# Optimization experiments

Measured on AMD Instinct MI355X. Metric: run time of the kernel, lower is better.

## Reference

```python
import jax, jax.numpy as jnp
import numpy as np
from jax import lax


def _binarize(t):
    # sign binarization to +1/-1 (zero maps to -1, matching torch.where(t > 0, 1, -1))
    return jnp.where(t > 0, 1.0, -1.0).astype(t.dtype)


def _bconv(x, w, b):
    # binary conv: binarize input and weights, then standard 3x3 'same' conv
    y = lax.conv_general_dilated(
        _binarize(x), _binarize(w),
        window_strides=(1, 1), padding=((1, 1), (1, 1)),
        dimension_numbers=('NCHW', 'OIHW', 'NCHW'))
    return y + b[None, :, None, None]


def _maxpool2(x):
    return lax.reduce_window(x, -jnp.inf, lax.max, (1, 1, 2, 2), (1, 1, 2, 2), 'VALID')


def setup_inputs() -> dict:
    key = jax.random.key(0)
    ks = jax.random.split(key, 13)
    s = 0.1
    return {
        'x': jax.random.normal(ks[0], (4096, 1, 28, 28), jnp.float32),
        'w1': jax.random.normal(ks[1], (32, 1, 3, 3), jnp.float32) * s,
        'b1': jax.random.normal(ks[2], (32,), jnp.float32) * s,
        'w2': jax.random.normal(ks[3], (64, 32, 3, 3), jnp.float32) * s,
        'b2': jax.random.normal(ks[4], (64,), jnp.float32) * s,
        'w3': jax.random.normal(ks[5], (16, 64, 3, 3), jnp.float32) * s,
        'b3': jax.random.normal(ks[6], (16,), jnp.float32) * s,
        'fc1_w': jax.random.normal(ks[7], (256, 16 * 7 * 7), jnp.float32) * s,
        'fc1_b': jax.random.normal(ks[8], (256,), jnp.float32) * s,
        'fc2_w': jax.random.normal(ks[9], (128, 256), jnp.float32) * s,
        'fc2_b': jax.random.normal(ks[10], (128,), jnp.float32) * s,
        'fc3_w': jax.random.normal(ks[11], (10, 128), jnp.float32) * s,
        'fc3_b': jax.random.normal(ks[12], (10,), jnp.float32) * s,
    }


def reference(x, w1, b1, w2, b2, w3, b3, fc1_w, fc1_b, fc2_w, fc2_b, fc3_w, fc3_b):
    h = jax.nn.relu(_maxpool2(_bconv(x, w1, b1)))      # [B,32,14,14]
    h = jax.nn.relu(_maxpool2(_bconv(h, w2, b2)))      # [B,64,7,7]
    h = jax.nn.relu(_bconv(h, w3, b3))                 # [B,16,7,7]
    h = h.reshape(-1, 16 * 7 * 7)
    h = jax.nn.relu(h @ fc1_w.T + fc1_b)
    h = jax.nn.relu(h @ fc2_w.T + fc2_b)
    return h @ fc3_w.T + fc3_b                          # [B,10]
```

## Files before the change

kernel.cpp:

```cpp
#include <hip/hip_runtime.h>
#include <cstdint>

#define OFF_PW    0
#define OFF_W1T   4096
#define OFF_W2T   823296
#define OFF_H3T   954368
#define OFF_H1T   14061568
#define OFF_H2T   18255872

__global__ __launch_bounds__(256) void prep(
    const float* __restrict__ w1, const float* __restrict__ w2,
    const float* __restrict__ w3,
    const float* __restrict__ fc1_w, const float* __restrict__ fc2_w,
    uint32_t* __restrict__ pw, float* __restrict__ w1T, float* __restrict__ w2T) {
    int t = threadIdx.x;
    if (blockIdx.x == 0) {
        if (t < 32) {
            uint32_t b = 0;
            for (int k = 0; k < 9; ++k) b |= (w1[t * 9 + k] > 0.f ? 1u : 0u) << k;
            pw[t] = b;
        }
        for (int idx = t; idx < 576; idx += 256) {
            int oc = idx / 9, tap = idx % 9;
            int kh = tap / 3, kw = tap % 3;
            uint32_t b = 0;
            for (int ic = 0; ic < 32; ++ic)
                b |= (w2[((oc * 32 + ic) * 3 + kh) * 3 + kw] > 0.f ? 1u : 0u) << ic;
            pw[32 + idx] = b;
        }
        for (int idx = t; idx < 144; idx += 256) {
            int oc = idx / 9, tap = idx % 9;
            int kh = tap / 3, kw = tap % 3;
            uint32_t lo = 0, hi = 0;
            for (int ic = 0; ic < 32; ++ic) {
                lo |= (w3[((oc * 64 + ic) * 3 + kh) * 3 + kw] > 0.f ? 1u : 0u) << ic;
                hi |= (w3[((oc * 64 + ic + 32) * 3 + kh) * 3 + kw] > 0.f ? 1u : 0u) << ic;
            }
            pw[608 + idx * 2] = lo;
            pw[608 + idx * 2 + 1] = hi;
        }
    } else {
        int e = (blockIdx.x - 1) * 256 + t;
        if (e < 204800) {
            int k = e >> 8, n = e & 255;
            w1T[e] = (k < 784) ? fc1_w[n * 784 + k] : 0.f;
        } else {
            int e2 = e - 204800;
            int k = e2 >> 7, n = e2 & 127;
            w2T[e2] = fc2_w[n * 256 + k];
        }
    }
}

__global__ __launch_bounds__(256) void conv_stack(
    const float* __restrict__ x,
    const float* __restrict__ b1, const float* __restrict__ b2,
    const float* __restrict__ b3,
    const uint32_t* __restrict__ pw,
    float* __restrict__ h3T) {
    __shared__ uint32_t s_wb1[32];
    __shared__ uint32_t s_W2[576];
    __shared__ uint32_t s_W3[288];
    __shared__ float s_b1[32], s_b2[64], s_b3[16];
    __shared__ uint32_t s_xrow[28];
    __shared__ uint32_t s_H1[256];
    __shared__ uint32_t s_H2[162];

    const int t = threadIdx.x;
    const int img = blockIdx.x;

    s_H1[t] = 0;
    if (t < 162) s_H2[t] = 0;
    if (t < 32) { s_wb1[t] = pw[t]; s_b1[t] = b1[t]; }
    if (t >= 32 && t < 96) s_b2[t - 32] = b2[t - 32];
    if (t >= 96 && t < 112) s_b3[t - 96] = b3[t - 96];
    for (int i = t; i < 576; i += 256) s_W2[i] = pw[32 + i];
    for (int i = t; i < 288; i += 256) s_W3[i] = pw[608 + i];
    if (t >= 192 && t < 220) {
        int r = t - 192;
        const float* xr = x + img * 784 + r * 28;
        uint32_t b = 0;
        for (int j = 0; j < 28; ++j) b |= (xr[j] > 0.f ? 1u : 0u) << j;
        s_xrow[r] = b;
    }
    __syncthreads();

    if (t < 196) {
        int pi = t / 14, pj = t % 14;
        uint32_t sarr[4], marr[4];
        int pcm[4];
#pragma unroll
        for (int p = 0; p < 4; ++p) {
            int i = 2 * pi + (p >> 1), j = 2 * pj + (p & 1);
            uint32_t sb = 0, mb = 0;
            int bit = 0;
#pragma unroll
            for (int di = -1; di <= 1; ++di) {
                int y = i + di;
                bool rv = (unsigned)y < 28u;
                uint32_t row = rv ? s_xrow[rv ? y : 0] : 0u;
#pragma unroll
                for (int dj = -1; dj <= 1; ++dj) {
                    int xx = j + dj;
                    bool v = rv && (unsigned)xx < 28u;
                    if (v) {
                        mb |= 1u << bit;
                        sb |= ((row >> xx) & 1u) << bit;
                    }
                    ++bit;
                }
            }
            sarr[p] = sb; marr[p] = mb; pcm[p] = __popc(mb);
        }
        uint32_t word = 0;
#pragma unroll
        for (int c = 0; c < 32; ++c) {
            uint32_t w = s_wb1[c];
            int best = -1000;
#pragma unroll
            for (int p = 0; p < 4; ++p) {
                int v = pcm[p] - 2 * __popc((sarr[p] ^ w) & marr[p]);
                best = v > best ? v : best;
            }
            word |= ((float)best + s_b1[c] > 0.f ? 1u : 0u) << c;
        }
        s_H1[(pi + 1) * 16 + (pj + 1)] = word;
    }
    __syncthreads();

    for (int task = t; task < 400; task += 256) {
        int q = task / 25, ip = task - q * 25;
        int pi = ip / 5 + 1, pj = ip % 5 + 1;
        uint32_t cell[16];
#pragma unroll
        for (int r = 0; r < 4; ++r)
#pragma unroll
            for (int c = 0; c < 4; ++c)
                cell[r * 4 + c] = s_H1[(2 * pi + r) * 16 + (2 * pj + c)];
        uint32_t nib = 0;
#pragma unroll
        for (int o = 0; o < 4; ++o) {
            int oc = q * 4 + o;
            const uint32_t* wrow = &s_W2[oc * 9];
            int best = -100000;
#pragma unroll
            for (int a = 0; a < 2; ++a)
#pragma unroll
                for (int b = 0; b < 2; ++b) {
                    int S = 0;
#pragma unroll
                    for (int kh = 0; kh < 3; ++kh)
#pragma unroll
                        for (int kw = 0; kw < 3; ++kw)
                            S += __popc(cell[(a + kh) * 4 + (b + kw)] ^ wrow[kh * 3 + kw]);
                    int v = 288 - 2 * S;
                    best = v > best ? v : best;
                }
            nib |= ((float)best + s_b2[oc] > 0.f ? 1u : 0u) << (oc & 31);
        }
        atomicOr((unsigned int*)&s_H2[((pi + 1) * 9 + (pj + 1)) * 2 + (q >> 3)],
                 (unsigned int)nib);
    }
    for (int task = t; task < 384; task += 256) {
        int q = task / 24, bp = task - q * 24;
        int pi, pj;
        if (bp < 7)       { pi = 0; pj = bp; }
        else if (bp < 14) { pi = 6; pj = bp - 7; }
        else if (bp < 19) { pi = bp - 13; pj = 0; }
        else              { pi = bp - 18; pj = 6; }
        uint32_t vr[4], vc[4];
#pragma unroll
        for (int r = 0; r < 4; ++r) {
            vr[r] = ((unsigned)(2 * pi - 1 + r) < 14u) ? 0xFFFFFFFFu : 0u;
            vc[r] = ((unsigned)(2 * pj - 1 + r) < 14u) ? 0xFFFFFFFFu : 0u;
        }
        uint32_t cell[16], V[16];
#pragma unroll
        for (int r = 0; r < 4; ++r)
#pragma unroll
            for (int c = 0; c < 4; ++c) {
                cell[r * 4 + c] = s_H1[(2 * pi + r) * 16 + (2 * pj + c)];
                V[r * 4 + c] = vr[r] & vc[c];
            }
        int nvp[4];
#pragma unroll
        for (int a = 0; a < 2; ++a)
#pragma unroll
            for (int b = 0; b < 2; ++b) {
                int i = 2 * pi + a, j = 2 * pj + b;
                int vy = 3 - (i == 0) - (i == 13);
                int vx = 3 - (j == 0) - (j == 13);
                nvp[a * 2 + b] = 32 * vy * vx;
            }
        uint32_t nib = 0;
#pragma unroll
        for (int o = 0; o < 4; ++o) {
            int oc = q * 4 + o;
            const uint32_t* wrow = &s_W2[oc * 9];
            int best = -100000;
#pragma unroll
            for (int a = 0; a < 2; ++a)
#pragma unroll
                for (int b = 0; b < 2; ++b) {
                    int S = 0;
#pragma unroll
                    for (int kh = 0; kh < 3; ++kh)
#pragma unroll
                        for (int kw = 0; kw < 3; ++kw) {
                            int ci = (a + kh) * 4 + (b + kw);
                            S += __popc((cell[ci] ^ wrow[kh * 3 + kw]) & V[ci]);
                        }
                    int v = nvp[a * 2 + b] - 2 * S;
                    best = v > best ? v : best;
                }
            nib |= ((float)best + s_b2[oc] > 0.f ? 1u : 0u) << (oc & 31);
        }
        atomicOr((unsigned int*)&s_H2[((pi + 1) * 9 + (pj + 1)) * 2 + (q >> 3)],
                 (unsigned int)nib);
    }
    __syncthreads();

    for (int task = t; task < 784; task += 256) {
        int oc = task / 49, pos = task - oc * 49;
        int pi = pos / 7, pj = pos % 7;
        uint32_t vr[3], vc[3];
#pragma unroll
        for (int d = 0; d < 3; ++d) {
            vr[d] = ((unsigned)(pi - 1 + d) < 7u) ? 0xFFFFFFFFu : 0u;
            vc[d] = ((unsigned)(pj - 1 + d) < 7u) ? 0xFFFFFFFFu : 0u;
        }
        int vy = 3 - (pi == 0) - (pi == 6);
        int vx = 3 - (pj == 0) - (pj == 6);
        int Nv = 64 * vy * vx;
        const uint32_t* wr = &s_W3[oc * 18];
        int S = 0;
#pragma unroll
        for (int kh = 0; kh < 3; ++kh)
#pragma unroll
            for (int kw = 0; kw < 3; ++kw) {
                uint32_t V = vr[kh] & vc[kw];
                int idx = ((pi + kh) * 9 + (pj + kw)) * 2;
                S += __popc((s_H2[idx] ^ wr[(kh * 3 + kw) * 2]) & V);
                S += __popc((s_H2[idx + 1] ^ wr[(kh * 3 + kw) * 2 + 1]) & V);
            }
        float h = (float)(Nv - 2 * S) + s_b3[oc];
        h3T[task * 4096 + img] = h > 0.f ? h : 0.f;
    }
}

__global__ __launch_bounds__(256) void fc1_gemm(
    const float* __restrict__ aT,
    const float* __restrict__ bT,
    const float* __restrict__ bias,
    float* __restrict__ oT) {
    const int KC = 80, LD = 68;
    __shared__ float As[KC * LD];
    __shared__ float Bs[KC * LD];
    const int t = threadIdx.x;
    const int tx = t & 15, ty = t >> 4;
    const int img0 = blockIdx.x * 64;
    const int n0 = blockIdx.y * 64;
    float acc[4][4] = {{0.f}};

    for (int kc = 0; kc < 800; kc += KC) {
#pragma unroll
        for (int s = 0; s < 5; ++s) {
            int v = t + s * 256;
            int kk = v >> 4, i4 = (v & 15) * 4;
            *(float4*)&As[kk * LD + i4] =
                *(const float4*)&aT[(kc + kk) * 4096 + img0 + i4];
            *(float4*)&Bs[kk * LD + i4] =
                *(const float4*)&bT[(kc + kk) * 256 + n0 + i4];
        }
        __syncthreads();
#pragma unroll 4
        for (int kk = 0; kk < KC; ++kk) {
            float4 a = *(const float4*)&As[kk * LD + ty * 4];
            float4 b = *(const float4*)&Bs[kk * LD + tx * 4];
            acc[0][0] += a.x * b.x; acc[0][1] += a.x * b.y;
            acc[0][2] += a.x * b.z; acc[0][3] += a.x * b.w;
            acc[1][0] += a.y * b.x; acc[1][1] += a.y * b.y;
            acc[1][2] += a.y * b.z; acc[1][3] += a.y * b.w;
            acc[2][0] += a.z * b.x; acc[2][1] += a.z * b.y;
            acc[2][2] += a.z * b.z; acc[2][3] += a.z * b.w;
            acc[3][0] += a.w * b.x; acc[3][1] += a.w * b.y;
            acc[3][2] += a.w * b.z; acc[3][3] += a.w * b.w;
        }
        __syncthreads();
    }
    float4 bb = *(const float4*)&bias[n0 + tx * 4];
    float bv[4] = {bb.x, bb.y, bb.z, bb.w};
#pragma unroll
    for (int jj = 0; jj < 4; ++jj) {
        float4 ov;
        ov.x = acc[0][jj] + bv[jj]; ov.x = ov.x > 0.f ? ov.x : 0.f;
        ov.y = acc[1][jj] + bv[jj]; ov.y = ov.y > 0.f ? ov.y : 0.f;
        ov.z = acc[2][jj] + bv[jj]; ov.z = ov.z > 0.f ? ov.z : 0.f;
        ov.w = acc[3][jj] + bv[jj]; ov.w = ov.w > 0.f ? ov.w : 0.f;
        *(float4*)&oT[(n0 + tx * 4 + jj) * 4096 + img0 + ty * 4] = ov;
    }
}

__global__ __launch_bounds__(256) void fc2_gemm(
    const float* __restrict__ aT,
    const float* __restrict__ bT,
    const float* __restrict__ bias,
    float* __restrict__ oT) {
    const int KC = 64, LDA = 68, LDB = 36;
    __shared__ float As[KC * LDA];
    __shared__ float Bs[KC * LDB];
    const int t = threadIdx.x;
    const int tx = t & 15, ty = t >> 4;
    const int img0 = blockIdx.x * 64;
    const int n0 = blockIdx.y * 32;
    float acc[4][2] = {{0.f}};

    for (int kc = 0; kc < 256; kc += KC) {
#pragma unroll
        for (int s = 0; s < 4; ++s) {
            int v = t + s * 256;
            int kk = v >> 4, i4 = (v & 15) * 4;
            *(float4*)&As[kk * LDA + i4] =
                *(const float4*)&aT[(kc + kk) * 4096 + img0 + i4];
        }
#pragma unroll
        for (int s = 0; s < 2; ++s) {
            int v = t + s * 256;
            int kk = v >> 3, n4 = (v & 7) * 4;
            *(float4*)&Bs[kk * LDB + n4] =
                *(const float4*)&bT[(kc + kk) * 128 + n0 + n4];
        }
        __syncthreads();
#pragma unroll 4
        for (int kk = 0; kk < KC; ++kk) {
            float4 a = *(const float4*)&As[kk * LDA + ty * 4];
            float2 b = *(const float2*)&Bs[kk * LDB + tx * 2];
            acc[0][0] += a.x * b.x; acc[0][1] += a.x * b.y;
            acc[1][0] += a.y * b.x; acc[1][1] += a.y * b.y;
            acc[2][0] += a.z * b.x; acc[2][1] += a.z * b.y;
            acc[3][0] += a.w * b.x; acc[3][1] += a.w * b.y;
        }
        __syncthreads();
    }
#pragma unroll
    for (int j = 0; j < 2; ++j) {
        int n = n0 + tx * 2 + j;
        float bj = bias[n];
        float4 ov;
        ov.x = acc[0][j] + bj; ov.x = ov.x > 0.f ? ov.x : 0.f;
        ov.y = acc[1][j] + bj; ov.y = ov.y > 0.f ? ov.y : 0.f;
        ov.z = acc[2][j] + bj; ov.z = ov.z > 0.f ? ov.z : 0.f;
        ov.w = acc[3][j] + bj; ov.w = ov.w > 0.f ? ov.w : 0.f;
        *(float4*)&oT[n * 4096 + img0 + ty * 4] = ov;
    }
}

__global__ __launch_bounds__(256) void fc3_gemm(
    const float* __restrict__ aT,
    const float* __restrict__ w,
    const float* __restrict__ bias,
    float* __restrict__ out) {
    int id = blockIdx.x * 256 + threadIdx.x;
    int n = id >> 12, img = id & 4095;
    const float* wr = w + n * 128;
    float a0 = 0.f, a1 = 0.f, a2 = 0.f, a3 = 0.f;
#pragma unroll 8
    for (int k = 0; k < 128; k += 4) {
        a0 += aT[(k + 0) * 4096 + img] * wr[k + 0];
        a1 += aT[(k + 1) * 4096 + img] * wr[k + 1];
        a2 += aT[(k + 2) * 4096 + img] * wr[k + 2];
        a3 += aT[(k + 3) * 4096 + img] * wr[k + 3];
    }
    out[img * 10 + n] = (a0 + a1) + (a2 + a3) + bias[n];
}

extern "C" void kernel_launch(void* const* d_in, const int* in_sizes, int n_in,
                              void* d_out, int out_size, void* d_ws, size_t ws_size,
                              hipStream_t stream) {
    const float* x     = (const float*)d_in[0];
    const float* w1    = (const float*)d_in[1];
    const float* b1    = (const float*)d_in[2];
    const float* w2    = (const float*)d_in[3];
    const float* b2    = (const float*)d_in[4];
    const float* w3    = (const float*)d_in[5];
    const float* b3    = (const float*)d_in[6];
    const float* fc1_w = (const float*)d_in[7];
    const float* fc1_b = (const float*)d_in[8];
    const float* fc2_w = (const float*)d_in[9];
    const float* fc2_b = (const float*)d_in[10];
    const float* fc3_w = (const float*)d_in[11];
    const float* fc3_b = (const float*)d_in[12];
    float* out = (float*)d_out;

    const int B = in_sizes[0] / 784;
    char* ws = (char*)d_ws;
    uint32_t* pw = (uint32_t*)(ws + OFF_PW);
    float* w1T = (float*)(ws + OFF_W1T);
    float* w2T = (float*)(ws + OFF_W2T);
    float* h3T = (float*)(ws + OFF_H3T);
    float* h1T = (float*)(ws + OFF_H1T);
    float* h2T = (float*)(ws + OFF_H2T);

    hipLaunchKernelGGL(prep, dim3(929), dim3(256), 0, stream,
                       w1, w2, w3, fc1_w, fc2_w, pw, w1T, w2T);
    hipLaunchKernelGGL(conv_stack, dim3(B), dim3(256), 0, stream,
                       x, b1, b2, b3, pw, h3T);
    hipLaunchKernelGGL(fc1_gemm, dim3(B / 64, 4), dim3(256), 0, stream,
                       h3T, w1T, fc1_b, h1T);
    hipLaunchKernelGGL(fc2_gemm, dim3(B / 64, 4), dim3(256), 0, stream,
                       h1T, w2T, fc2_b, h2T);
    hipLaunchKernelGGL(fc3_gemm, dim3(B * 10 / 256), dim3(256), 0, stream,
                       h2T, fc3_w, fc3_b, out);
}
```

Baseline: 219.7 us.

## Process one image per wavefront in conv stack with padded bit layout and precomputed thresholds

The conv stack now maps one image to each 64-lane wavefront, four images per block, each with its own padded bit buffers in shared memory. Conv1 reads bits from a zero-padded row layout, and conv2 gives one output channel to each lane with register-held weights, packing results with a ballot instead of shared atomics. Bias comparisons become integer thresholds, and border padding corrections come from tables built in prep. The table lives in the h1T workspace region, which fc1 later overwrites. Interior tiles run fewer bitwise ops, but wavefronts loop sequentially over positions.

```diff
diff --git a/kernel.cpp b/kernel.cpp
--- a/kernel.cpp
+++ b/kernel.cpp
@@ -1,24 +1,45 @@
 #include <hip/hip_runtime.h>
 #include <cstdint>
 
-#define OFF_PW    0
 #define OFF_W1T   4096
 #define OFF_W2T   823296
 #define OFF_H3T   954368
 #define OFF_H1T   14061568
 #define OFF_H2T   18255872
 
+#define TW_WB1    0
+#define TW_W2     32
+#define TW_W3     608
+#define TW_CORR2  896
+#define TW_CORR3  1920
+#define TW_TLE1   2176
+#define TW_TGE1   2208
+#define TW_TLE2   2240
+#define TW_TGE2   2304
+
+__device__ __forceinline__ int imin2(int a, int b) { return a < b ? a : b; }
+__device__ __forceinline__ int imax2(int a, int b) { return a > b ? a : b; }
+
 __global__ __launch_bounds__(256) void prep(
-    const float* __restrict__ w1, const float* __restrict__ w2,
+    const float* __restrict__ w1, const float* __restrict__ b1,
+    const float* __restrict__ w2, const float* __restrict__ b2,
     const float* __restrict__ w3,
     const float* __restrict__ fc1_w, const float* __restrict__ fc2_w,
-    uint32_t* __restrict__ pw, float* __restrict__ w1T, float* __restrict__ w2T) {
+    int* __restrict__ tab, float* __restrict__ w1T, float* __restrict__ w2T) {
     int t = threadIdx.x;
+    uint32_t* utab = (uint32_t*)tab;
     if (blockIdx.x == 0) {
         if (t < 32) {
             uint32_t b = 0;
             for (int k = 0; k < 9; ++k) b |= (w1[t * 9 + k] > 0.f ? 1u : 0u) << k;
-            pw[t] = b;
+            utab[TW_WB1 + t] = b;
+            tab[TW_TLE1 + t] = (int)floorf((9.f + b1[t]) * 0.5f);
+            tab[TW_TGE1 + t] = (int)floorf(-b1[t]) + 1;
+        }
+        if (t >= 32 && t < 96) {
+            int oc = t - 32;
+            tab[TW_TLE2 + oc] = (int)floorf((288.f + b2[oc]) * 0.5f);
+            tab[TW_TGE2 + oc] = (int)floorf(-b2[oc]) + 1;
         }
         for (int idx = t; idx < 576; idx += 256) {
             int oc = idx / 9, tap = idx % 9;
@@ -26,18 +47,46 @@
             uint32_t b = 0;
             for (int ic = 0; ic < 32; ++ic)
                 b |= (w2[((oc * 32 + ic) * 3 + kh) * 3 + kw] > 0.f ? 1u : 0u) << ic;
-            pw[32 + idx] = b;
-        }
-        for (int idx = t; idx < 144; idx += 256) {
-            int oc = idx / 9, tap = idx % 9;
+            utab[TW_W2 + idx] = b;
+        }
+        for (int idx = t; idx < 288; idx += 256) {
+            int oc = idx / 18, rem = idx % 18;
+            int tap = rem >> 1, word = rem & 1;
             int kh = tap / 3, kw = tap % 3;
-            uint32_t lo = 0, hi = 0;
-            for (int ic = 0; ic < 32; ++ic) {
-                lo |= (w3[((oc * 64 + ic) * 3 + kh) * 3 + kw] > 0.f ? 1u : 0u) << ic;
-                hi |= (w3[((oc * 64 + ic + 32) * 3 + kh) * 3 + kw] > 0.f ? 1u : 0u) << ic;
-            }
-            pw[608 + idx * 2] = lo;
-            pw[608 + idx * 2 + 1] = hi;
+            uint32_t b = 0;
+            for (int ic = 0; ic < 32; ++ic)
+                b |= (w3[((oc * 64 + ic + 32 * word) * 3 + kh) * 3 + kw] > 0.f ? 1u : 0u) << ic;
+            utab[TW_W3 + idx] = b;
+        }
+        __syncthreads();
+        for (int idx = t; idx < 1024; idx += 256) {
+            int pat = idx >> 6, oc = idx & 63;
+            int s = 0, n = 0;
+            for (int tap = 0; tap < 9; ++tap) {
+                int kh = tap / 3, kw = tap % 3;
+                bool pad = ((pat & 1) && kh == 0) || ((pat & 2) && kh == 2) ||
+                           ((pat & 4) && kw == 0) || ((pat & 8) && kw == 2);
+                if (pad) { s += __popc(utab[TW_W2 + oc * 9 + tap]); ++n; }
+            }
+            tab[TW_CORR2 + idx] = 2 * s - 32 * n;
+        }
+        {
+            int idx = t;
+            if (idx < 256) {
+                int pat = idx >> 4, oc = idx & 15;
+                int s = 0, n = 0;
+                for (int tap = 0; tap < 9; ++tap) {
+                    int kh = tap / 3, kw = tap % 3;
+                    bool pad = ((pat & 1) && kh == 0) || ((pat & 2) && kh == 2) ||
+                               ((pat & 4) && kw == 0) || ((pat & 8) && kw == 2);
+                    if (pad) {
+                        s += __popc(utab[TW_W3 + oc * 18 + tap * 2]) +
+                             __popc(utab[TW_W3 + oc * 18 + tap * 2 + 1]);
+                        ++n;
+                    }
+                }
+                tab[TW_CORR3 + idx] = 2 * s - 64 * n;
+            }
         }
     } else {
         int e = (blockIdx.x - 1) * 256 + t;
@@ -52,199 +101,236 @@
     }
 }
 
-__global__ __launch_bounds__(256) void conv_stack(
+#define WV_SIZE 456
+
+__global__ __launch_bounds__(256, 6) void conv_stack(
     const float* __restrict__ x,
-    const float* __restrict__ b1, const float* __restrict__ b2,
     const float* __restrict__ b3,
-    const uint32_t* __restrict__ pw,
+    const int* __restrict__ tab,
     float* __restrict__ h3T) {
-    __shared__ uint32_t s_wb1[32];
-    __shared__ uint32_t s_W2[576];
-    __shared__ uint32_t s_W3[288];
-    __shared__ float s_b1[32], s_b2[64], s_b3[16];
-    __shared__ uint32_t s_xrow[28];
-    __shared__ uint32_t s_H1[256];
-    __shared__ uint32_t s_H2[162];
-
+    __shared__ uint32_t SH[4 * WV_SIZE];
     const int t = threadIdx.x;
-    const int img = blockIdx.x;
-
-    s_H1[t] = 0;
-    if (t < 162) s_H2[t] = 0;
-    if (t < 32) { s_wb1[t] = pw[t]; s_b1[t] = b1[t]; }
-    if (t >= 32 && t < 96) s_b2[t - 32] = b2[t - 32];
-    if (t >= 96 && t < 112) s_b3[t - 96] = b3[t - 96];
-    for (int i = t; i < 576; i += 256) s_W2[i] = pw[32 + i];
-    for (int i = t; i < 288; i += 256) s_W3[i] = pw[608 + i];
-    if (t >= 192 && t < 220) {
-        int r = t - 192;
-        const float* xr = x + img * 784 + r * 28;
+    const int wid = t >> 6, lane = t & 63;
+    const int img = blockIdx.x * 4 + wid;
+    uint32_t* W = SH + wid * WV_SIZE;
+    const uint32_t* utab = (const uint32_t*)tab;
+
+#pragma unroll
+    for (int k = 0; k < 8; ++k) {
+        int idx = lane + k * 64;
+        if (idx < WV_SIZE) W[idx] = 0;
+    }
+
+    if (lane < 28) {
+        const float* xr = x + img * 784 + lane * 28;
         uint32_t b = 0;
-        for (int j = 0; j < 28; ++j) b |= (xr[j] > 0.f ? 1u : 0u) << j;
-        s_xrow[r] = b;
+#pragma unroll
+        for (int q = 0; q < 7; ++q) {
+            float4 v = *(const float4*)(xr + q * 4);
+            b |= (v.x > 0.f ? 1u : 0u) << (q * 4 + 0);
+            b |= (v.y > 0.f ? 1u : 0u) << (q * 4 + 1);
+            b |= (v.z > 0.f ? 1u : 0u) << (q * 4 + 2);
+            b |= (v.w > 0.f ? 1u : 0u) << (q * 4 + 3);
+        }
+        W[1 + lane] = b << 1;
     }
     __syncthreads();
 
-    if (t < 196) {
-        int pi = t / 14, pj = t % 14;
-        uint32_t sarr[4], marr[4];
+    for (int it = 0; it < 3; ++it) {
+        int p = it * 64 + lane;
+        bool act = p < 144;
+        int pp = act ? p : 0;
+        int Pi = 1 + pp / 12, Pj = 1 + pp % 12;
+        int i0 = 2 * Pi, j0 = 2 * Pj;
+        uint32_t r0 = W[i0], r1 = W[i0 + 1], r2 = W[i0 + 2], r3 = W[i0 + 3];
+        uint32_t f0a = (r0 >> j0) & 7, f0b = (r0 >> (j0 + 1)) & 7;
+        uint32_t f1a = (r1 >> j0) & 7, f1b = (r1 >> (j0 + 1)) & 7;
+        uint32_t f2a = (r2 >> j0) & 7, f2b = (r2 >> (j0 + 1)) & 7;
+        uint32_t f3a = (r3 >> j0) & 7, f3b = (r3 >> (j0 + 1)) & 7;
+        uint32_t s00 = f0a | (f1a << 3) | (f2a << 6);
+        uint32_t s01 = f0b | (f1b << 3) | (f2b << 6);
+        uint32_t s10 = f1a | (f2a << 3) | (f3a << 6);
+        uint32_t s11 = f1b | (f2b << 3) | (f3b << 6);
+        uint32_t word = 0;
+#pragma unroll
+        for (int oc = 0; oc < 32; ++oc) {
+            uint32_t w = utab[TW_WB1 + oc];
+            int m0 = __popc(s00 ^ w), m1 = __popc(s01 ^ w);
+            int m2 = __popc(s10 ^ w), m3 = __popc(s11 ^ w);
+            int mn = imin2(imin2(m0, m1), imin2(m2, m3));
+            word |= (mn <= tab[TW_TLE1 + oc] ? 1u : 0u) << oc;
+        }
+        if (act) W[32 + (Pi + 1) * 16 + (Pj + 1)] = word;
+    }
+    {
+        int p = lane;
+        bool act = p < 52;
+        int pp = act ? p : 28;
+        int Pi, Pj;
+        if (pp < 14)      { Pi = 0;  Pj = pp; }
+        else if (pp < 28) { Pi = 13; Pj = pp - 14; }
+        else if (pp < 40) { Pi = pp - 28 + 1; Pj = 0; }
+        else              { Pi = pp - 40 + 1; Pj = 13; }
+        int i0 = 2 * Pi, j0 = 2 * Pj;
+        uint32_t r0 = W[i0], r1 = W[i0 + 1], r2 = W[i0 + 2], r3 = W[i0 + 3];
+        uint32_t f0a = (r0 >> j0) & 7, f0b = (r0 >> (j0 + 1)) & 7;
+        uint32_t f1a = (r1 >> j0) & 7, f1b = (r1 >> (j0 + 1)) & 7;
+        uint32_t f2a = (r2 >> j0) & 7, f2b = (r2 >> (j0 + 1)) & 7;
+        uint32_t f3a = (r3 >> j0) & 7, f3b = (r3 >> (j0 + 1)) & 7;
+        uint32_t smp[4];
+        smp[0] = f0a | (f1a << 3) | (f2a << 6);
+        smp[1] = f0b | (f1b << 3) | (f2b << 6);
+        smp[2] = f1a | (f2a << 3) | (f3a << 6);
+        smp[3] = f1b | (f2b << 3) | (f3b << 6);
+        uint32_t mb[4];
         int pcm[4];
 #pragma unroll
-        for (int p = 0; p < 4; ++p) {
-            int i = 2 * pi + (p >> 1), j = 2 * pj + (p & 1);
-            uint32_t sb = 0, mb = 0;
-            int bit = 0;
-#pragma unroll
-            for (int di = -1; di <= 1; ++di) {
-                int y = i + di;
-                bool rv = (unsigned)y < 28u;
-                uint32_t row = rv ? s_xrow[rv ? y : 0] : 0u;
-#pragma unroll
-                for (int dj = -1; dj <= 1; ++dj) {
-                    int xx = j + dj;
-                    bool v = rv && (unsigned)xx < 28u;
-                    if (v) {
-                        mb |= 1u << bit;
-                        sb |= ((row >> xx) & 1u) << bit;
+        for (int a = 0; a < 2; ++a) {
+            int i = 2 * Pi + a;
+            uint32_t vre = 0x1FF;
+            if (i == 0)  vre &= ~0x007u;
+            if (i == 27) vre &= ~0x1C0u;
+#pragma unroll
+            for (int bb = 0; bb < 2; ++bb) {
+                int j = 2 * Pj + bb;
+                uint32_t vce = 0x1FF;
+                if (j == 0)  vce &= ~0x049u;
+                if (j == 27) vce &= ~0x124u;
+                mb[a * 2 + bb] = vre & vce;
+                pcm[a * 2 + bb] = __popc(vre & vce);
+            }
+        }
+        uint32_t word = 0;
+#pragma unroll
+        for (int oc = 0; oc < 32; ++oc) {
+            uint32_t w = utab[TW_WB1 + oc];
+            int best = -1000;
+#pragma unroll
+            for (int p4 = 0; p4 < 4; ++p4) {
+                int v = pcm[p4] - 2 * __popc((smp[p4] ^ w) & mb[p4]);
+                best = imax2(best, v);
+            }
+            word |= (best >= tab[TW_TGE1 + oc] ? 1u : 0u) << oc;
+        }
+        if (act) W[32 + (Pi + 1) * 16 + (Pj + 1)] = word;
+    }
+    __syncthreads();
+
+    {
+        uint32_t w2r[9];
+#pragma unroll
+        for (int k = 0; k < 9; ++k) w2r[k] = utab[TW_W2 + lane * 9 + k];
+        const int tle2 = tab[TW_TLE2 + lane];
+        const int tge2 = tab[TW_TGE2 + lane];
+        const uint32_t* H1 = W + 32;
+        uint32_t* H2 = W + 288;
+
+        for (int Pi = 1; Pi <= 5; ++Pi) {
+            for (int Pj = 1; Pj <= 5; ++Pj) {
+                uint32_t c[16];
+#pragma unroll
+                for (int r = 0; r < 4; ++r) {
+                    uint2 lo = *(const uint2*)&H1[(2 * Pi + r) * 16 + 2 * Pj];
+                    uint2 hi = *(const uint2*)&H1[(2 * Pi + r) * 16 + 2 * Pj + 2];
+                    c[r * 4 + 0] = lo.x; c[r * 4 + 1] = lo.y;
+                    c[r * 4 + 2] = hi.x; c[r * 4 + 3] = hi.y;
+                }
+                int Sv[4];
+#pragma unroll
+                for (int a = 0; a < 2; ++a)
+#pragma unroll
+                    for (int bb = 0; bb < 2; ++bb) {
+                        int s = 0;
+#pragma unroll
+                        for (int kh = 0; kh < 3; ++kh)
+#pragma unroll
+                            for (int kw = 0; kw < 3; ++kw)
+                                s += __popc(c[(a + kh) * 4 + (bb + kw)] ^ w2r[kh * 3 + kw]);
+                        Sv[a * 2 + bb] = s;
                     }
-                    ++bit;
+                int mn = imin2(imin2(Sv[0], Sv[1]), imin2(Sv[2], Sv[3]));
+                uint64_t bal = __ballot(mn <= tle2);
+                if (lane == 0) {
+                    uint2 wv = make_uint2((uint32_t)bal, (uint32_t)(bal >> 32));
+                    *(uint2*)&H2[((Pi + 1) * 9 + (Pj + 1)) * 2] = wv;
                 }
             }
-            sarr[p] = sb; marr[p] = mb; pcm[p] = __popc(mb);
-        }
-        uint32_t word = 0;
-#pragma unroll
-        for (int c = 0; c < 32; ++c) {
-            uint32_t w = s_wb1[c];
-            int best = -1000;
-#pragma unroll
-            for (int p = 0; p < 4; ++p) {
-                int v = pcm[p] - 2 * __popc((sarr[p] ^ w) & marr[p]);
-                best = v > best ? v : best;
-            }
-            word |= ((float)best + s_b1[c] > 0.f ? 1u : 0u) << c;
-        }
-        s_H1[(pi + 1) * 16 + (pj + 1)] = word;
+        }
+        for (int bp = 0; bp < 24; ++bp) {
+            int Pi, Pj;
+            if (bp < 7)       { Pi = 0; Pj = bp; }
+            else if (bp < 14) { Pi = 6; Pj = bp - 7; }
+            else if (bp < 19) { Pi = bp - 14 + 1; Pj = 0; }
+            else              { Pi = bp - 19 + 1; Pj = 6; }
+            uint32_t c[16];
+#pragma unroll
+            for (int r = 0; r < 4; ++r) {
+                uint2 lo = *(const uint2*)&H1[(2 * Pi + r) * 16 + 2 * Pj];
+                uint2 hi = *(const uint2*)&H1[(2 * Pi + r) * 16 + 2 * Pj + 2];
+                c[r * 4 + 0] = lo.x; c[r * 4 + 1] = lo.y;
+                c[r * 4 + 2] = hi.x; c[r * 4 + 3] = hi.y;
+            }
+            int Sv[4];
+#pragma unroll
+            for (int a = 0; a < 2; ++a)
+#pragma unroll
+                for (int bb = 0; bb < 2; ++bb) {
+                    int s = 0;
+#pragma unroll
+                    for (int kh = 0; kh < 3; ++kh)
+#pragma unroll
+                        for (int kw = 0; kw < 3; ++kw)
+                            s += __popc(c[(a + kh) * 4 + (bb + kw)] ^ w2r[kh * 3 + kw]);
+                    Sv[a * 2 + bb] = s;
+                }
+            int best = -100000;
+#pragma unroll
+            for (int a = 0; a < 2; ++a)
+#pragma unroll
+                for (int bb = 0; bb < 2; ++bb) {
+                    int i = 2 * Pi + a, j = 2 * Pj + bb;
+                    int pat = (i == 0 ? 1 : 0) | (i == 13 ? 2 : 0) |
+                              (j == 0 ? 4 : 0) | (j == 13 ? 8 : 0);
+                    int D = 288 - 2 * Sv[a * 2 + bb] + tab[TW_CORR2 + pat * 64 + lane];
+                    best = imax2(best, D);
+                }
+            uint64_t bal = __ballot(best >= tge2);
+            if (lane == 0) {
+                uint2 wv = make_uint2((uint32_t)bal, (uint32_t)(bal >> 32));
+                *(uint2*)&H2[((Pi + 1) * 9 + (Pj + 1)) * 2] = wv;
+            }
+        }
     }
     __syncthreads();
 
-    for (int task = t; task < 400; task += 256) {
-        int q = task / 25, ip = task - q * 25;
-        int pi = ip / 5 + 1, pj = ip % 5 + 1;
-        uint32_t cell[16];
-#pragma unroll
-        for (int r = 0; r < 4; ++r)
-#pragma unroll
-            for (int c = 0; c < 4; ++c)
-                cell[r * 4 + c] = s_H1[(2 * pi + r) * 16 + (2 * pj + c)];
-        uint32_t nib = 0;
-#pragma unroll
-        for (int o = 0; o < 4; ++o) {
-            int oc = q * 4 + o;
-            const uint32_t* wrow = &s_W2[oc * 9];
-            int best = -100000;
-#pragma unroll
-            for (int a = 0; a < 2; ++a)
-#pragma unroll
-                for (int b = 0; b < 2; ++b) {
-                    int S = 0;
-#pragma unroll
-                    for (int kh = 0; kh < 3; ++kh)
-#pragma unroll
-                        for (int kw = 0; kw < 3; ++kw)
-                            S += __popc(cell[(a + kh) * 4 + (b + kw)] ^ wrow[kh * 3 + kw]);
-                    int v = 288 - 2 * S;
-                    best = v > best ? v : best;
+    {
+        const uint32_t* H2 = W + 288;
+        int oc = lane & 15, sub = lane >> 4;
+        uint32_t w3r[18];
+#pragma unroll
+        for (int k = 0; k < 18; ++k) w3r[k] = utab[TW_W3 + oc * 18 + k];
+        float bias3 = b3[oc];
+        for (int g = 0; g < 13; ++g) {
+            int pos = g * 4 + sub;
+            bool act = pos < 49;
+            int pp = act ? pos : 0;
+            int Pi = pp / 7, Pj = pp % 7;
+            int s = 0;
+#pragma unroll
+            for (int kh = 0; kh < 3; ++kh)
+#pragma unroll
+                for (int kw = 0; kw < 3; ++kw) {
+                    uint2 hv = *(const uint2*)&H2[((Pi + kh) * 9 + (Pj + kw)) * 2];
+                    s += __popc(hv.x ^ w3r[(kh * 3 + kw) * 2]) +
+                         __popc(hv.y ^ w3r[(kh * 3 + kw) * 2 + 1]);
                 }
-            nib |= ((float)best + s_b2[oc] > 0.f ? 1u : 0u) << (oc & 31);
-        }
-        atomicOr((unsigned int*)&s_H2[((pi + 1) * 9 + (pj + 1)) * 2 + (q >> 3)],
-                 (unsigned int)nib);
-    }
-    for (int task = t; task < 384; task += 256) {
-        int q = task / 24, bp = task - q * 24;
-        int pi, pj;
-        if (bp < 7)       { pi = 0; pj = bp; }
-        else if (bp < 14) { pi = 6; pj = bp - 7; }
-        else if (bp < 19) { pi = bp - 13; pj = 0; }
-        else              { pi = bp - 18; pj = 6; }
-        uint32_t vr[4], vc[4];
-#pragma unroll
-        for (int r = 0; r < 4; ++r) {
-            vr[r] = ((unsigned)(2 * pi - 1 + r) < 14u) ? 0xFFFFFFFFu : 0u;
-            vc[r] = ((unsigned)(2 * pj - 1 + r) < 14u) ? 0xFFFFFFFFu : 0u;
-        }
-        uint32_t cell[16], V[16];
-#pragma unroll
-        for (int r = 0; r < 4; ++r)
-#pragma unroll
-            for (int c = 0; c < 4; ++c) {
-                cell[r * 4 + c] = s_H1[(2 * pi + r) * 16 + (2 * pj + c)];
-                V[r * 4 + c] = vr[r] & vc[c];
-            }
-        int nvp[4];
-#pragma unroll
-        for (int a = 0; a < 2; ++a)
-#pragma unroll
-            for (int b = 0; b < 2; ++b) {
-                int i = 2 * pi + a, j = 2 * pj + b;
-                int vy = 3 - (i == 0) - (i == 13);
-                int vx = 3 - (j == 0) - (j == 13);
-                nvp[a * 2 + b] = 32 * vy * vx;
-            }
-        uint32_t nib = 0;
-#pragma unroll
-        for (int o = 0; o < 4; ++o) {
-            int oc = q * 4 + o;
-            const uint32_t* wrow = &s_W2[oc * 9];
-            int best = -100000;
-#pragma unroll
-            for (int a = 0; a < 2; ++a)
-#pragma unroll
-                for (int b = 0; b < 2; ++b) {
-                    int S = 0;
-#pragma unroll
-                    for (int kh = 0; kh < 3; ++kh)
-#pragma unroll
-                        for (int kw = 0; kw < 3; ++kw) {
-                            int ci = (a + kh) * 4 + (b + kw);
-                            S += __popc((cell[ci] ^ wrow[kh * 3 + kw]) & V[ci]);
-                        }
-                    int v = nvp[a * 2 + b] - 2 * S;
-                    best = v > best ? v : best;
-                }
-            nib |= ((float)best + s_b2[oc] > 0.f ? 1u : 0u) << (oc & 31);
-        }
-        atomicOr((unsigned int*)&s_H2[((pi + 1) * 9 + (pj + 1)) * 2 + (q >> 3)],
-                 (unsigned int)nib);
-    }
-    __syncthreads();
-
-    for (int task = t; task < 784; task += 256) {
-        int oc = task / 49, pos = task - oc * 49;
-        int pi = pos / 7, pj = pos % 7;
-        uint32_t vr[3], vc[3];
-#pragma unroll
-        for (int d = 0; d < 3; ++d) {
-            vr[d] = ((unsigned)(pi - 1 + d) < 7u) ? 0xFFFFFFFFu : 0u;
-            vc[d] = ((unsigned)(pj - 1 + d) < 7u) ? 0xFFFFFFFFu : 0u;
-        }
-        int vy = 3 - (pi == 0) - (pi == 6);
-        int vx = 3 - (pj == 0) - (pj == 6);
-        int Nv = 64 * vy * vx;
-        const uint32_t* wr = &s_W3[oc * 18];
-        int S = 0;
-#pragma unroll
-        for (int kh = 0; kh < 3; ++kh)
-#pragma unroll
-            for (int kw = 0; kw < 3; ++kw) {
-                uint32_t V = vr[kh] & vc[kw];
-                int idx = ((pi + kh) * 9 + (pj + kw)) * 2;
-                S += __popc((s_H2[idx] ^ wr[(kh * 3 + kw) * 2]) & V);
-                S += __popc((s_H2[idx + 1] ^ wr[(kh * 3 + kw) * 2 + 1]) & V);
-            }
-        float h = (float)(Nv - 2 * S) + s_b3[oc];
-        h3T[task * 4096 + img] = h > 0.f ? h : 0.f;
+            int pat = (Pi == 0 ? 1 : 0) | (Pi == 6 ? 2 : 0) |
+                      (Pj == 0 ? 4 : 0) | (Pj == 6 ? 8 : 0);
+            int D = 576 - 2 * s + tab[TW_CORR3 + pat * 16 + oc];
+            float h = (float)D + bias3;
+            h = h > 0.f ? h : 0.f;
+            if (act) h3T[(oc * 49 + pp) * 4096 + img] = h;
+        }
     }
 }
 
@@ -394,17 +480,17 @@
 
     const int B = in_sizes[0] / 784;
     char* ws = (char*)d_ws;
-    uint32_t* pw = (uint32_t*)(ws + OFF_PW);
     float* w1T = (float*)(ws + OFF_W1T);
     float* w2T = (float*)(ws + OFF_W2T);
     float* h3T = (float*)(ws + OFF_H3T);
     float* h1T = (float*)(ws + OFF_H1T);
     float* h2T = (float*)(ws + OFF_H2T);
+    int* tab = (int*)(ws + OFF_H1T);
 
     hipLaunchKernelGGL(prep, dim3(929), dim3(256), 0, stream,
-                       w1, w2, w3, fc1_w, fc2_w, pw, w1T, w2T);
-    hipLaunchKernelGGL(conv_stack, dim3(B), dim3(256), 0, stream,
-                       x, b1, b2, b3, pw, h3T);
+                       w1, b1, w2, b2, w3, fc1_w, fc2_w, tab, w1T, w2T);
+    hipLaunchKernelGGL(conv_stack, dim3(B / 4), dim3(256), 0, stream,
+                       x, b3, tab, h3T);
     hipLaunchKernelGGL(fc1_gemm, dim3(B / 64, 4), dim3(256), 0, stream,
                        h3T, w1T, fc1_b, h1T);
     hipLaunchKernelGGL(fc2_gemm, dim3(B / 64, 4), dim3(256), 0, stream,
```

After: 207.9 us. 5.4% less time.
